# Performance work log

Measured on AMD Instinct MI355X. Metric: run time of the kernel, lower is better.

Reference implementation:

```python
import jax, jax.numpy as jnp
import numpy as np
from functools import partial

B = 524288      # batch
CH = 30         # channel_num (input dim)
FEA = 42        # feature dim consumed by all classifiers
HID = 64        # assumed hidden width of the (unshown) Feature MLP
NC = 2          # num_class -> number of conditional-domain experts
ND = 6          # num_domain
ALPHA = 1.0

# Gradient Reversal Layer: identity fwd, -alpha * grad bwd
@partial(jax.custom_vjp, nondiff_argnums=(1,))
def grl(x, alpha):
    return x

def _grl_fwd(x, alpha):
    return x, None

def _grl_bwd(alpha, res, g):
    return (-alpha * g,)

grl.defvjp(_grl_fwd, _grl_bwd)


def setup_inputs() -> dict:
    key = jax.random.key(0)
    ks = jax.random.split(key, 24)
    r = lambda k, shape, s=0.1: (jax.random.normal(k, shape, dtype=jnp.float32) * s)
    inp = {
        "x": jax.random.normal(ks[0], (B, CH), dtype=jnp.float32),
        "y": jax.random.randint(ks[1], (B,), 0, NC, dtype=jnp.int32),
        # Feature MLP (assumed: CH -> HID -> FEA with ReLU)
        "W_f1": r(ks[2], (CH, HID)), "b_f1": jnp.zeros((HID,), jnp.float32),
        "W_f2": r(ks[3], (HID, FEA)), "b_f2": jnp.zeros((FEA,), jnp.float32),
        # TaskClassifier: 42 -> 20 -> NC
        "W_t1": r(ks[4], (FEA, 20)), "b_t1": jnp.zeros((20,), jnp.float32),
        "W_t2": r(ks[5], (20, NC)), "b_t2": jnp.zeros((NC,), jnp.float32),
        # prior domain classifier: 42 -> 20 -> 20 -> ND
        "W_p1": r(ks[6], (FEA, 20)), "b_p1": jnp.zeros((20,), jnp.float32),
        "W_p2": r(ks[7], (20, 20)), "b_p2": jnp.zeros((20,), jnp.float32),
        "W_p3": r(ks[8], (20, ND)), "b_p3": jnp.zeros((ND,), jnp.float32),
        # NC conditional domain experts, stacked: [NC, ...]
        "W_c1": r(ks[9], (NC, FEA, 20)), "b_c1": jnp.zeros((NC, 20), jnp.float32),
        "W_c2": r(ks[10], (NC, 20, 20)), "b_c2": jnp.zeros((NC, 20), jnp.float32),
        "W_c3": r(ks[11], (NC, 20, ND)), "b_c3": jnp.zeros((NC, ND), jnp.float32),
    }
    return inp


def reference(x, y, W_f1, b_f1, W_f2, b_f2, W_t1, b_t1, W_t2, b_t2,
              W_p1, b_p1, W_p2, b_p2, W_p3, b_p3,
              W_c1, b_c1, W_c2, b_c2, W_c3, b_c3):
    # feature extractor
    h = jax.nn.relu(x @ W_f1 + b_f1)
    fea = jax.nn.relu(h @ W_f2 + b_f2)              # [B, 42]
    # task head
    t = jax.nn.relu(fea @ W_t1 + b_t1)
    task_predict = t @ W_t2 + b_t2                   # [B, NC]
    # gradient-reversed feature for domain heads
    fr = grl(fea, ALPHA)
    # prior domain classifier
    p = jax.nn.relu(fr @ W_p1 + b_p1)
    p = jax.nn.relu(p @ W_p2 + b_p2)
    pd_predict = p @ W_p3 + b_p3                     # [B, ND]
    # conditional experts: with NC=2 compute all experts, then route by label
    c = jax.nn.relu(jnp.einsum('bf,cfh->bch', fr, W_c1) + b_c1[None])
    c = jax.nn.relu(jnp.einsum('bch,chk->bck', c, W_c2) + b_c2[None])
    cd_all = jnp.einsum('bck,ckd->bcd', c, W_c3) + b_c3[None]   # [B, NC, ND]
    cd_predicts = jnp.take_along_axis(cd_all, y[:, None, None].astype(jnp.int32), axis=1)[:, 0, :]
    return (task_predict, pd_predict, cd_predicts)
```

## Files before the change

kernel.cpp:

```cpp
#include <hip/hip_runtime.h>
#include <hip/hip_bf16.h>

typedef __bf16 bf8 __attribute__((ext_vector_type(8)));
typedef unsigned short u16x8 __attribute__((ext_vector_type(8)));
typedef float f32x4 __attribute__((ext_vector_type(4)));
typedef float f32x2 __attribute__((ext_vector_type(2)));
typedef unsigned int u32x4 __attribute__((ext_vector_type(4)));

union FragU { u16x8 u; bf8 b; u32x4 q; };
union BiasU { f32x4 f; u32x4 q; };

struct __attribute__((packed, aligned(4))) F4u { float v[4]; };
struct __attribute__((packed, aligned(4))) F2u { float v[2]; };

static __device__ __forceinline__ f32x4 MM(const FragU& a, const FragU& b, f32x4 c) {
  return __builtin_amdgcn_mfma_f32_16x16x32_bf16(a.b, b.b, c, 0, 0, 0);
}

#define NBATCH 524288
#define NTIL (NBATCH / 128)
#define GRID 512
#define NFRAG 37

__global__ __launch_bounds__(64) void cdann_prep(
    const float* __restrict__ gWf1, const float* __restrict__ gbf1,
    const float* __restrict__ gWf2, const float* __restrict__ gbf2,
    const float* __restrict__ gWt1, const float* __restrict__ gbt1,
    const float* __restrict__ gWt2, const float* __restrict__ gbt2,
    const float* __restrict__ gWp1, const float* __restrict__ gbp1,
    const float* __restrict__ gWp2, const float* __restrict__ gbp2,
    const float* __restrict__ gWp3, const float* __restrict__ gbp3,
    const float* __restrict__ gWc1, const float* __restrict__ gbc1,
    const float* __restrict__ gWc2, const float* __restrict__ gbc2,
    const float* __restrict__ gWc3, const float* __restrict__ gbc3,
    u32x4* __restrict__ ws)
{
  const int lane = (int)threadIdx.x & 63;
  const int fid = (int)blockIdx.x;
  const int g = lane >> 4;
  const int c15 = lane & 15;

  auto colF2 = [](int nt, int m) -> int {
    if (nt < 2) return 8 * (m >> 2) + 4 * nt + (m & 3);
    const int gm = m >> 2, r = m & 3;
    if (gm == 0) return 32 + r;
    if (gm == 1) return 36 + r;
    if (gm == 2 && r < 2) return 40 + r;
    return -1;
  };

  if (fid >= 34) {
    const int nt = fid - 34;
    BiasU b;
#pragma unroll
    for (int r = 0; r < 4; ++r) {
      const int col = colF2(nt, g * 4 + r);
      b.f[r] = (col >= 0) ? gbf2[col] : 0.f;
    }
    ws[fid * 64 + lane] = b.q;
    return;
  }

  auto v_f1 = [&](int k, int m, int nt) -> float {
    const int n = 32 * (nt >> 1) + 8 * (m >> 2) + 4 * (nt & 1) + (m & 3);
    if (k < 30) return gWf1[k * 64 + n];
    if (k == 30) return gbf1[n];
    return 0.f;
  };
  auto v_f2 = [&](int k, int m, int nt) -> float {
    const int col = colF2(nt, m);
    return (col >= 0) ? gWf2[k * 42 + col] : 0.f;
  };
  auto ffea = [](int v) -> int {
    if (v < 36) return v;
    if (v == 36) return -2;
    if (v >= 40 && v <= 43) return v - 4;
    if (v == 48 || v == 49) return v - 8;
    return -1;
  };
  auto v_q = [&](int k, int m, int nt) -> float {
    const int i = ffea(k);
    if (i == -1) return 0.f;
    const int gm = m >> 2;
    const int u = 4 * nt + (m & 3);
    const int head = u / 5;
    const int f = 5 * gm + (u % 5);
    if (head == 0) return (i == -2) ? gbt1[f] : gWt1[i * 20 + f];
    if (head == 1) return (i == -2) ? gbp1[f] : gWp1[i * 20 + f];
    if (head == 2) return (i == -2) ? gbc1[f] : gWc1[i * 20 + f];
    return (i == -2) ? gbc1[20 + f] : gWc1[(42 + i) * 20 + f];
  };
  auto v_tp = [&](int k, int m, int nt) -> float {
    const int ks = k >> 5, j = k & 7, gk = (k >> 3) & 3;
    const int gm = m >> 2;
    const int u = 4 * nt + (m & 3);
    const int isP2 = (u < 5);
    const int cp = 5 * gm + u;
    const int isT2 = (!isP2 && gm == 0 && (u == 5 || u == 6));
    const int ct = u - 5;
    if (ks == 0) {
      if (j < 5) { const int i = 5 * gk + j; return isT2 ? gWt2[i * 2 + ct] : 0.f; }
      if (j == 7 && gk == 0) { if (isT2) return gbt2[ct]; if (isP2) return gbp2[cp]; }
      return 0.f;
    } else {
      if (j < 5) { const int i = 5 * gk + j; return isP2 ? gWp2[i * 20 + cp] : 0.f; }
      return 0.f;
    }
  };
  auto v_cc = [&](int k, int m, int nt) -> float {
    const int ks = k >> 5, j = k & 7, gk = (k >> 3) & 3;
    const int gm = m >> 2;
    const int u = 4 * nt + (m & 3);
    const int isE0 = (u < 5);
    const int isE1 = (u >= 5 && u < 10);
    const int c0 = 5 * gm + u;
    const int c1 = 5 * gm + (u - 5);
    if (ks == 0) {
      if (j < 5) { const int i = 5 * gk + j; return isE0 ? gWc2[i * 20 + c0] : 0.f; }
      if (j == 7 && gk == 0) { if (isE0) return gbc2[c0]; if (isE1) return gbc2[20 + c1]; }
      return 0.f;
    } else {
      if (j < 5) { const int i = 5 * gk + j; return isE1 ? gWc2[(20 + i) * 20 + c1] : 0.f; }
      return 0.f;
    }
  };
  auto v_o = [&](int k, int m, int nt) -> float {
    const int ks = k >> 5, j = k & 7, gk = (k >> 3) & 3;
    const int gm = m >> 2, r = m & 3;
    int kind = -1, c = 0;
    if (nt == 0) {
      if (gm == 0) { kind = 0; c = r; }
      else if (gm == 1) { if (r < 2) { kind = 0; c = 4 + r; } else { kind = 1; c = r - 2; } }
      else if (gm == 2) { kind = 1; c = 2 + r; }
      else { kind = 2; c = r; }
    } else {
      if (gm == 0 && r < 2) { kind = 2; c = 4 + r; }
    }
    if (kind < 0) return 0.f;
    if (ks == 0) {
      if (j < 5) { const int i = 5 * gk + j; return (kind == 0) ? gWp3[i * 6 + c] : 0.f; }
      if (j < 7) { const int i = 5 * gk + (j - 5); return (kind == 2) ? gWc3[(20 + i) * 6 + c] : 0.f; }
      if (gk == 0) {
        if (kind == 0) return gbp3[c];
        if (kind == 1) return gbc3[c];
        return gbc3[6 + c];
      }
      return 0.f;
    } else {
      if (j < 5) { const int i = 5 * gk + j; return (kind == 1) ? gWc3[i * 6 + c] : 0.f; }
      const int i = 5 * gk + 2 + (j - 5);
      return (kind == 2) ? gWc3[(20 + i) * 6 + c] : 0.f;
    }
  };

  int ks, nt, which;
  if (fid < 4)       { ks = 0;                nt = fid;            which = 0; }
  else if (fid < 10) { int t = fid - 4;  ks = t / 3; nt = t % 3;   which = 1; }
  else if (fid < 20) { int t = fid - 10; ks = t / 5; nt = t % 5;   which = 2; }
  else if (fid < 24) { int t = fid - 20; ks = t / 2; nt = t % 2;   which = 3; }
  else if (fid < 30) { int t = fid - 24; ks = t / 3; nt = t % 3;   which = 4; }
  else               { int t = fid - 30; ks = t / 2; nt = t % 2;   which = 5; }

  FragU f;
#pragma unroll
  for (int j = 0; j < 8; ++j) {
    const int k = ks * 32 + g * 8 + j;
    float v;
    switch (which) {
      case 0: v = v_f1(k, c15, nt); break;
      case 1: v = v_f2(k, c15, nt); break;
      case 2: v = v_q(k, c15, nt); break;
      case 3: v = v_tp(k, c15, nt); break;
      case 4: v = v_cc(k, c15, nt); break;
      default: v = v_o(k, c15, nt); break;
    }
    f.b[j] = (__bf16)v;
  }
  ws[fid * 64 + lane] = f.q;
}

__global__ __launch_bounds__(256, 2) void cdann_fwd(
    const float* __restrict__ gx, const int* __restrict__ gy,
    const u32x4* __restrict__ ws, float* __restrict__ gout)
{
  const int tid = (int)threadIdx.x;
  const int lane = tid & 63;
  const int w = tid >> 6;
  const int g = lane >> 4;
  const int c15 = lane & 15;

  FragU wF1[4], wF2[2][3], wQ[2][5], wTP[2][2], wCC[2][3], wO[2][2];
#pragma unroll
  for (int nt = 0; nt < 4; ++nt) wF1[nt].q = ws[nt * 64 + lane];
#pragma unroll
  for (int ks = 0; ks < 2; ++ks) {
#pragma unroll
    for (int nt = 0; nt < 3; ++nt) wF2[ks][nt].q = ws[(4 + ks * 3 + nt) * 64 + lane];
#pragma unroll
    for (int nt = 0; nt < 5; ++nt) wQ[ks][nt].q = ws[(10 + ks * 5 + nt) * 64 + lane];
#pragma unroll
    for (int nt = 0; nt < 2; ++nt) wTP[ks][nt].q = ws[(20 + ks * 2 + nt) * 64 + lane];
#pragma unroll
    for (int nt = 0; nt < 3; ++nt) wCC[ks][nt].q = ws[(24 + ks * 3 + nt) * 64 + lane];
#pragma unroll
    for (int nt = 0; nt < 2; ++nt) wO[ks][nt].q = ws[(30 + ks * 2 + nt) * 64 + lane];
  }
  f32x4 bF2[3];
#pragma unroll
  for (int nt = 0; nt < 3; ++nt) {
    BiasU b; b.q = ws[(34 + nt) * 64 + lane];
    bF2[nt] = b.f;
  }

#pragma unroll
  for (int nt = 0; nt < 4; ++nt) asm volatile("" : "+v"(wF1[nt].u));
#pragma unroll
  for (int ks = 0; ks < 2; ++ks) {
#pragma unroll
    for (int nt = 0; nt < 3; ++nt) asm volatile("" : "+v"(wF2[ks][nt].u));
#pragma unroll
    for (int nt = 0; nt < 5; ++nt) asm volatile("" : "+v"(wQ[ks][nt].u));
#pragma unroll
    for (int nt = 0; nt < 2; ++nt) asm volatile("" : "+v"(wTP[ks][nt].u));
#pragma unroll
    for (int nt = 0; nt < 3; ++nt) asm volatile("" : "+v"(wCC[ks][nt].u));
#pragma unroll
    for (int nt = 0; nt < 2; ++nt) asm volatile("" : "+v"(wO[ks][nt].u));
  }
#pragma unroll
  for (int nt = 0; nt < 3; ++nt) asm volatile("" : "+v"(bF2[nt]));

  const f32x4 zf = {0.f, 0.f, 0.f, 0.f};
  const __bf16 one = (__bf16)1.0f;
  const __bf16 zero = (__bf16)0.0f;
  float* const outT = gout;
  float* const outP = gout + (size_t)2 * NBATCH;
  float* const outC = gout + (size_t)8 * NBATCH;

  auto chain = [&](const FragU& bx, int s, int y) {
    f32x4 aH[4];
#pragma unroll
    for (int nt = 0; nt < 4; ++nt) aH[nt] = MM(wF1[nt], bx, zf);
    FragU bh0, bh1;
#pragma unroll
    for (int j = 0; j < 8; ++j) {
      bh0.b[j] = (__bf16)fmaxf(aH[j >> 2][j & 3], 0.f);
      bh1.b[j] = (__bf16)fmaxf(aH[2 + (j >> 2)][j & 3], 0.f);
    }
    f32x4 aF[3];
#pragma unroll
    for (int nt = 0; nt < 3; ++nt) aF[nt] = MM(wF2[1][nt], bh1, MM(wF2[0][nt], bh0, zf));
    FragU bf0, bf1;
#pragma unroll
    for (int j = 0; j < 8; ++j)
      bf0.b[j] = (__bf16)fmaxf(aF[j >> 2][j & 3] + bF2[j >> 2][j & 3], 0.f);
#pragma unroll
    for (int j = 0; j < 4; ++j)
      bf1.b[j] = (__bf16)fmaxf(aF[2][j] + bF2[2][j], 0.f);
    bf1.b[4] = (g == 0) ? one : zero;
    bf1.b[5] = zero; bf1.b[6] = zero; bf1.b[7] = zero;
    f32x4 aQ[5];
#pragma unroll
    for (int nt = 0; nt < 5; ++nt) aQ[nt] = MM(wQ[1][nt], bf1, MM(wQ[0][nt], bf0, zf));
    auto rq = [&](int u) { return (__bf16)fmaxf(aQ[u >> 2][u & 3], 0.f); };
    FragU tp0, tp1, cc0, cc1;
#pragma unroll
    for (int j = 0; j < 5; ++j) {
      tp0.b[j] = rq(j);
      tp1.b[j] = rq(5 + j);
      cc0.b[j] = rq(10 + j);
      cc1.b[j] = rq(15 + j);
    }
    tp0.b[5] = zero; tp0.b[6] = zero; tp0.b[7] = (g == 0) ? one : zero;
    tp1.b[5] = zero; tp1.b[6] = zero; tp1.b[7] = zero;
    cc0.b[5] = zero; cc0.b[6] = zero; cc0.b[7] = (g == 0) ? one : zero;
    cc1.b[5] = zero; cc1.b[6] = zero; cc1.b[7] = zero;
    f32x4 aT[2], aC[3];
#pragma unroll
    for (int nt = 0; nt < 2; ++nt) aT[nt] = MM(wTP[1][nt], tp1, MM(wTP[0][nt], tp0, zf));
#pragma unroll
    for (int nt = 0; nt < 3; ++nt) aC[nt] = MM(wCC[1][nt], cc1, MM(wCC[0][nt], cc0, zf));
    FragU f50, f51;
#pragma unroll
    for (int j = 0; j < 4; ++j) {
      f50.b[j] = (__bf16)fmaxf(aT[0][j], 0.f);
      f51.b[j] = (__bf16)fmaxf(aC[0][j], 0.f);
    }
    f50.b[4] = (__bf16)fmaxf(aT[1][0], 0.f);
    f50.b[5] = (__bf16)fmaxf(aC[1][1], 0.f);
    f50.b[6] = (__bf16)fmaxf(aC[1][2], 0.f);
    f50.b[7] = (g == 0) ? one : zero;
    f51.b[4] = (__bf16)fmaxf(aC[1][0], 0.f);
    f51.b[5] = (__bf16)fmaxf(aC[1][3], 0.f);
    f51.b[6] = (__bf16)fmaxf(aC[2][0], 0.f);
    f51.b[7] = (__bf16)fmaxf(aC[2][1], 0.f);
    f32x4 aO[2];
#pragma unroll
    for (int nt = 0; nt < 2; ++nt) aO[nt] = MM(wO[1][nt], f51, MM(wO[0][nt], f50, zf));
    if (g == 0) {
      f32x2 t2v = {aT[1][1], aT[1][2]};
      *(f32x2*)(outT + (size_t)s * 2) = t2v;
      f32x2 pa = {aO[0][0], aO[0][1]}, pb = {aO[0][2], aO[0][3]};
      *(f32x2*)(outP + (size_t)s * 6) = pa;
      *(f32x2*)(outP + (size_t)s * 6 + 2) = pb;
      if (y) { f32x2 cv = {aO[1][0], aO[1][1]}; *(f32x2*)(outC + (size_t)s * 6 + 4) = cv; }
    } else if (g == 1) {
      f32x2 pc = {aO[0][0], aO[0][1]};
      *(f32x2*)(outP + (size_t)s * 6 + 4) = pc;
      if (!y) { f32x2 cv = {aO[0][2], aO[0][3]}; *(f32x2*)(outC + (size_t)s * 6) = cv; }
    } else if (g == 2) {
      if (!y) {
        f32x2 ca = {aO[0][0], aO[0][1]}, cb = {aO[0][2], aO[0][3]};
        *(f32x2*)(outC + (size_t)s * 6 + 2) = ca;
        *(f32x2*)(outC + (size_t)s * 6 + 4) = cb;
      }
    } else {
      if (y) {
        f32x2 ca = {aO[0][0], aO[0][1]}, cb = {aO[0][2], aO[0][3]};
        *(f32x2*)(outC + (size_t)s * 6) = ca;
        *(f32x2*)(outC + (size_t)s * 6 + 2) = cb;
      }
    }
  };

  float xrA[8], xrB[8];
  int yA, yB;
  auto loadx = [&](int it) {
    const int sA = it * 128 + w * 16 + c15;
    const float* xpA = gx + (size_t)sA * 30 + g * 8;
    const float* xpB = xpA + (size_t)64 * 30;
    if (g < 3) {
      F4u a0 = *(const F4u*)xpA; F4u a1 = *(const F4u*)(xpA + 4);
      F4u b0 = *(const F4u*)xpB; F4u b1 = *(const F4u*)(xpB + 4);
#pragma unroll
      for (int j = 0; j < 4; ++j) {
        xrA[j] = a0.v[j]; xrA[4 + j] = a1.v[j];
        xrB[j] = b0.v[j]; xrB[4 + j] = b1.v[j];
      }
    } else {
      F4u a0 = *(const F4u*)xpA; F2u a1 = *(const F2u*)(xpA + 4);
      F4u b0 = *(const F4u*)xpB; F2u b1 = *(const F2u*)(xpB + 4);
#pragma unroll
      for (int j = 0; j < 4; ++j) { xrA[j] = a0.v[j]; xrB[j] = b0.v[j]; }
      xrA[4] = a1.v[0]; xrA[5] = a1.v[1]; xrA[6] = 1.0f; xrA[7] = 0.0f;
      xrB[4] = b1.v[0]; xrB[5] = b1.v[1]; xrB[6] = 1.0f; xrB[7] = 0.0f;
    }
    yA = gy[sA]; yB = gy[sA + 64];
  };

  int it = (int)blockIdx.x;
  loadx(it);

  while (it < NTIL) {
    const int nit = it + GRID;
    const int sgA = it * 128 + w * 16 + c15;
    const int sgB = sgA + 64;
    const int ysA = yA, ysB = yB;

    FragU bxA, bxB;
#pragma unroll
    for (int j = 0; j < 8; ++j) { bxA.b[j] = (__bf16)xrA[j]; bxB.b[j] = (__bf16)xrB[j]; }

    if (nit < NTIL) loadx(nit);

    chain(bxA, sgA, ysA);
    chain(bxB, sgB, ysB);

    it = nit;
  }
}

extern "C" void kernel_launch(void* const* d_in, const int* in_sizes, int n_in,
                              void* d_out, int out_size, void* d_ws, size_t ws_size,
                              hipStream_t stream) {
  (void)in_sizes; (void)n_in; (void)ws_size; (void)out_size;
  const float* gx  = (const float*)d_in[0];
  const int*   gy  = (const int*)d_in[1];
  const float* Wf1 = (const float*)d_in[2];  const float* bf1 = (const float*)d_in[3];
  const float* Wf2 = (const float*)d_in[4];  const float* bf2 = (const float*)d_in[5];
  const float* Wt1 = (const float*)d_in[6];  const float* bt1 = (const float*)d_in[7];
  const float* Wt2 = (const float*)d_in[8];  const float* bt2 = (const float*)d_in[9];
  const float* Wp1 = (const float*)d_in[10]; const float* bp1 = (const float*)d_in[11];
  const float* Wp2 = (const float*)d_in[12]; const float* bp2 = (const float*)d_in[13];
  const float* Wp3 = (const float*)d_in[14]; const float* bp3 = (const float*)d_in[15];
  const float* Wc1 = (const float*)d_in[16]; const float* bc1 = (const float*)d_in[17];
  const float* Wc2 = (const float*)d_in[18]; const float* bc2 = (const float*)d_in[19];
  const float* Wc3 = (const float*)d_in[20]; const float* bc3 = (const float*)d_in[21];
  float* out = (float*)d_out;
  u32x4* ws = (u32x4*)d_ws;

  cdann_prep<<<dim3(NFRAG), dim3(64), 0, stream>>>(
      Wf1, bf1, Wf2, bf2, Wt1, bt1, Wt2, bt2,
      Wp1, bp1, Wp2, bp2, Wp3, bp3, Wc1, bc1, Wc2, bc2, Wc3, bc3, ws);

  cdann_fwd<<<dim3(GRID), dim3(256), 0, stream>>>(gx, gy, ws, out);
}
```

Measured before the change: 36.29 us.

## Interleave four independent MFMA chains per stage and drop software prefetch

The main kernel now handles four 16-sample chunks per tile and runs each layer stage across all four chunks before moving to the next layer. This exposes independent MFMA chains to hide MFMA latency and dependency stalls. The cross-iteration x prefetch is replaced by loading all chunks at the top of each iteration. The grid doubles and the iteration count is fixed at compile time. Register pressure rises from keeping four chunks' fragments live, and load latency is no longer overlapped with the previous tile's compute.

```diff
diff --git a/kernel.cpp b/kernel.cpp
--- a/kernel.cpp
+++ b/kernel.cpp
@@ -18,8 +18,11 @@
 }
 
 #define NBATCH 524288
-#define NTIL (NBATCH / 128)
-#define GRID 512
+#define NCH 4
+#define SPB (NCH * 16 * 4)
+#define NTIL (NBATCH / SPB)
+#define GRID 1024
+#define ITERS (NTIL / GRID)
 #define NFRAG 37
 
 __global__ __launch_bounds__(64) void cdann_prep(
@@ -237,136 +240,137 @@
   float* const outP = gout + (size_t)2 * NBATCH;
   float* const outC = gout + (size_t)8 * NBATCH;
 
-  auto chain = [&](const FragU& bx, int s, int y) {
-    f32x4 aH[4];
-#pragma unroll
-    for (int nt = 0; nt < 4; ++nt) aH[nt] = MM(wF1[nt], bx, zf);
-    FragU bh0, bh1;
-#pragma unroll
-    for (int j = 0; j < 8; ++j) {
-      bh0.b[j] = (__bf16)fmaxf(aH[j >> 2][j & 3], 0.f);
-      bh1.b[j] = (__bf16)fmaxf(aH[2 + (j >> 2)][j & 3], 0.f);
-    }
-    f32x4 aF[3];
-#pragma unroll
-    for (int nt = 0; nt < 3; ++nt) aF[nt] = MM(wF2[1][nt], bh1, MM(wF2[0][nt], bh0, zf));
-    FragU bf0, bf1;
-#pragma unroll
-    for (int j = 0; j < 8; ++j)
-      bf0.b[j] = (__bf16)fmaxf(aF[j >> 2][j & 3] + bF2[j >> 2][j & 3], 0.f);
-#pragma unroll
-    for (int j = 0; j < 4; ++j)
-      bf1.b[j] = (__bf16)fmaxf(aF[2][j] + bF2[2][j], 0.f);
-    bf1.b[4] = (g == 0) ? one : zero;
-    bf1.b[5] = zero; bf1.b[6] = zero; bf1.b[7] = zero;
-    f32x4 aQ[5];
-#pragma unroll
-    for (int nt = 0; nt < 5; ++nt) aQ[nt] = MM(wQ[1][nt], bf1, MM(wQ[0][nt], bf0, zf));
-    auto rq = [&](int u) { return (__bf16)fmaxf(aQ[u >> 2][u & 3], 0.f); };
-    FragU tp0, tp1, cc0, cc1;
-#pragma unroll
-    for (int j = 0; j < 5; ++j) {
-      tp0.b[j] = rq(j);
-      tp1.b[j] = rq(5 + j);
-      cc0.b[j] = rq(10 + j);
-      cc1.b[j] = rq(15 + j);
-    }
-    tp0.b[5] = zero; tp0.b[6] = zero; tp0.b[7] = (g == 0) ? one : zero;
-    tp1.b[5] = zero; tp1.b[6] = zero; tp1.b[7] = zero;
-    cc0.b[5] = zero; cc0.b[6] = zero; cc0.b[7] = (g == 0) ? one : zero;
-    cc1.b[5] = zero; cc1.b[6] = zero; cc1.b[7] = zero;
-    f32x4 aT[2], aC[3];
-#pragma unroll
-    for (int nt = 0; nt < 2; ++nt) aT[nt] = MM(wTP[1][nt], tp1, MM(wTP[0][nt], tp0, zf));
-#pragma unroll
-    for (int nt = 0; nt < 3; ++nt) aC[nt] = MM(wCC[1][nt], cc1, MM(wCC[0][nt], cc0, zf));
-    FragU f50, f51;
-#pragma unroll
-    for (int j = 0; j < 4; ++j) {
-      f50.b[j] = (__bf16)fmaxf(aT[0][j], 0.f);
-      f51.b[j] = (__bf16)fmaxf(aC[0][j], 0.f);
-    }
-    f50.b[4] = (__bf16)fmaxf(aT[1][0], 0.f);
-    f50.b[5] = (__bf16)fmaxf(aC[1][1], 0.f);
-    f50.b[6] = (__bf16)fmaxf(aC[1][2], 0.f);
-    f50.b[7] = (g == 0) ? one : zero;
-    f51.b[4] = (__bf16)fmaxf(aC[1][0], 0.f);
-    f51.b[5] = (__bf16)fmaxf(aC[1][3], 0.f);
-    f51.b[6] = (__bf16)fmaxf(aC[2][0], 0.f);
-    f51.b[7] = (__bf16)fmaxf(aC[2][1], 0.f);
-    f32x4 aO[2];
-#pragma unroll
-    for (int nt = 0; nt < 2; ++nt) aO[nt] = MM(wO[1][nt], f51, MM(wO[0][nt], f50, zf));
-    if (g == 0) {
-      f32x2 t2v = {aT[1][1], aT[1][2]};
-      *(f32x2*)(outT + (size_t)s * 2) = t2v;
-      f32x2 pa = {aO[0][0], aO[0][1]}, pb = {aO[0][2], aO[0][3]};
-      *(f32x2*)(outP + (size_t)s * 6) = pa;
-      *(f32x2*)(outP + (size_t)s * 6 + 2) = pb;
-      if (y) { f32x2 cv = {aO[1][0], aO[1][1]}; *(f32x2*)(outC + (size_t)s * 6 + 4) = cv; }
-    } else if (g == 1) {
-      f32x2 pc = {aO[0][0], aO[0][1]};
-      *(f32x2*)(outP + (size_t)s * 6 + 4) = pc;
-      if (!y) { f32x2 cv = {aO[0][2], aO[0][3]}; *(f32x2*)(outC + (size_t)s * 6) = cv; }
-    } else if (g == 2) {
-      if (!y) {
-        f32x2 ca = {aO[0][0], aO[0][1]}, cb = {aO[0][2], aO[0][3]};
-        *(f32x2*)(outC + (size_t)s * 6 + 2) = ca;
-        *(f32x2*)(outC + (size_t)s * 6 + 4) = cb;
-      }
-    } else {
-      if (y) {
-        f32x2 ca = {aO[0][0], aO[0][1]}, cb = {aO[0][2], aO[0][3]};
-        *(f32x2*)(outC + (size_t)s * 6) = ca;
-        *(f32x2*)(outC + (size_t)s * 6 + 2) = cb;
-      }
-    }
-  };
-
-  float xrA[8], xrB[8];
-  int yA, yB;
-  auto loadx = [&](int it) {
-    const int sA = it * 128 + w * 16 + c15;
-    const float* xpA = gx + (size_t)sA * 30 + g * 8;
-    const float* xpB = xpA + (size_t)64 * 30;
-    if (g < 3) {
-      F4u a0 = *(const F4u*)xpA; F4u a1 = *(const F4u*)(xpA + 4);
-      F4u b0 = *(const F4u*)xpB; F4u b1 = *(const F4u*)(xpB + 4);
+  for (int ii = 0; ii < ITERS; ++ii) {
+    const int it = (int)blockIdx.x + ii * GRID;
+    const int base = it * SPB + w * (NCH * 16) + c15;
+
+    float xr[NCH][8];
+    int ys[NCH];
+#pragma unroll
+    for (int c = 0; c < NCH; ++c) {
+      const int s = base + c * 16;
+      const float* xp = gx + (size_t)s * 30 + g * 8;
+      if (g < 3) {
+        F4u a0 = *(const F4u*)xp; F4u a1 = *(const F4u*)(xp + 4);
+#pragma unroll
+        for (int j = 0; j < 4; ++j) { xr[c][j] = a0.v[j]; xr[c][4 + j] = a1.v[j]; }
+      } else {
+        F4u a0 = *(const F4u*)xp; F2u a1 = *(const F2u*)(xp + 4);
+#pragma unroll
+        for (int j = 0; j < 4; ++j) xr[c][j] = a0.v[j];
+        xr[c][4] = a1.v[0]; xr[c][5] = a1.v[1];
+        xr[c][6] = 1.0f; xr[c][7] = 0.0f;
+      }
+      ys[c] = gy[s];
+    }
+
+    FragU bh0[NCH], bh1[NCH];
+#pragma unroll
+    for (int c = 0; c < NCH; ++c) {
+      FragU bx;
+#pragma unroll
+      for (int j = 0; j < 8; ++j) bx.b[j] = (__bf16)xr[c][j];
+      f32x4 aH[4];
+#pragma unroll
+      for (int nt = 0; nt < 4; ++nt) aH[nt] = MM(wF1[nt], bx, zf);
+#pragma unroll
+      for (int j = 0; j < 8; ++j) {
+        bh0[c].b[j] = (__bf16)fmaxf(aH[j >> 2][j & 3], 0.f);
+        bh1[c].b[j] = (__bf16)fmaxf(aH[2 + (j >> 2)][j & 3], 0.f);
+      }
+    }
+
+    FragU bf0[NCH], bf1[NCH];
+#pragma unroll
+    for (int c = 0; c < NCH; ++c) {
+      f32x4 aF[3];
+#pragma unroll
+      for (int nt = 0; nt < 3; ++nt) aF[nt] = MM(wF2[1][nt], bh1[c], MM(wF2[0][nt], bh0[c], zf));
+#pragma unroll
+      for (int j = 0; j < 8; ++j)
+        bf0[c].b[j] = (__bf16)fmaxf(aF[j >> 2][j & 3] + bF2[j >> 2][j & 3], 0.f);
+#pragma unroll
+      for (int j = 0; j < 4; ++j)
+        bf1[c].b[j] = (__bf16)fmaxf(aF[2][j] + bF2[2][j], 0.f);
+      bf1[c].b[4] = (g == 0) ? one : zero;
+      bf1[c].b[5] = zero; bf1[c].b[6] = zero; bf1[c].b[7] = zero;
+    }
+
+    f32x4 aOr0[NCH], aOr1[NCH];
+    f32x2 t2v[NCH];
+#pragma unroll
+    for (int c = 0; c < NCH; ++c) {
+      f32x4 aQ[5];
+#pragma unroll
+      for (int nt = 0; nt < 5; ++nt) aQ[nt] = MM(wQ[1][nt], bf1[c], MM(wQ[0][nt], bf0[c], zf));
+      auto rq = [&](int u) { return (__bf16)fmaxf(aQ[u >> 2][u & 3], 0.f); };
+      FragU tp0, tp1, cc0, cc1;
+#pragma unroll
+      for (int j = 0; j < 5; ++j) {
+        tp0.b[j] = rq(j);
+        tp1.b[j] = rq(5 + j);
+        cc0.b[j] = rq(10 + j);
+        cc1.b[j] = rq(15 + j);
+      }
+      tp0.b[5] = zero; tp0.b[6] = zero; tp0.b[7] = (g == 0) ? one : zero;
+      tp1.b[5] = zero; tp1.b[6] = zero; tp1.b[7] = zero;
+      cc0.b[5] = zero; cc0.b[6] = zero; cc0.b[7] = (g == 0) ? one : zero;
+      cc1.b[5] = zero; cc1.b[6] = zero; cc1.b[7] = zero;
+      f32x4 aT[2], aC[3];
+#pragma unroll
+      for (int nt = 0; nt < 2; ++nt) aT[nt] = MM(wTP[1][nt], tp1, MM(wTP[0][nt], tp0, zf));
+#pragma unroll
+      for (int nt = 0; nt < 3; ++nt) aC[nt] = MM(wCC[1][nt], cc1, MM(wCC[0][nt], cc0, zf));
+      FragU f50, f51;
 #pragma unroll
       for (int j = 0; j < 4; ++j) {
-        xrA[j] = a0.v[j]; xrA[4 + j] = a1.v[j];
-        xrB[j] = b0.v[j]; xrB[4 + j] = b1.v[j];
-      }
-    } else {
-      F4u a0 = *(const F4u*)xpA; F2u a1 = *(const F2u*)(xpA + 4);
-      F4u b0 = *(const F4u*)xpB; F2u b1 = *(const F2u*)(xpB + 4);
-#pragma unroll
-      for (int j = 0; j < 4; ++j) { xrA[j] = a0.v[j]; xrB[j] = b0.v[j]; }
-      xrA[4] = a1.v[0]; xrA[5] = a1.v[1]; xrA[6] = 1.0f; xrA[7] = 0.0f;
-      xrB[4] = b1.v[0]; xrB[5] = b1.v[1]; xrB[6] = 1.0f; xrB[7] = 0.0f;
-    }
-    yA = gy[sA]; yB = gy[sA + 64];
-  };
-
-  int it = (int)blockIdx.x;
-  loadx(it);
-
-  while (it < NTIL) {
-    const int nit = it + GRID;
-    const int sgA = it * 128 + w * 16 + c15;
-    const int sgB = sgA + 64;
-    const int ysA = yA, ysB = yB;
-
-    FragU bxA, bxB;
-#pragma unroll
-    for (int j = 0; j < 8; ++j) { bxA.b[j] = (__bf16)xrA[j]; bxB.b[j] = (__bf16)xrB[j]; }
-
-    if (nit < NTIL) loadx(nit);
-
-    chain(bxA, sgA, ysA);
-    chain(bxB, sgB, ysB);
-
-    it = nit;
+        f50.b[j] = (__bf16)fmaxf(aT[0][j], 0.f);
+        f51.b[j] = (__bf16)fmaxf(aC[0][j], 0.f);
+      }
+      f50.b[4] = (__bf16)fmaxf(aT[1][0], 0.f);
+      f50.b[5] = (__bf16)fmaxf(aC[1][1], 0.f);
+      f50.b[6] = (__bf16)fmaxf(aC[1][2], 0.f);
+      f50.b[7] = (g == 0) ? one : zero;
+      f51.b[4] = (__bf16)fmaxf(aC[1][0], 0.f);
+      f51.b[5] = (__bf16)fmaxf(aC[1][3], 0.f);
+      f51.b[6] = (__bf16)fmaxf(aC[2][0], 0.f);
+      f51.b[7] = (__bf16)fmaxf(aC[2][1], 0.f);
+      aOr0[c] = MM(wO[0][0], f50, zf);
+      aOr0[c] = MM(wO[1][0], f51, aOr0[c]);
+      aOr1[c] = MM(wO[0][1], f50, zf);
+      aOr1[c] = MM(wO[1][1], f51, aOr1[c]);
+      t2v[c][0] = aT[1][1]; t2v[c][1] = aT[1][2];
+    }
+
+#pragma unroll
+    for (int c = 0; c < NCH; ++c) {
+      const int s = base + c * 16;
+      const int y = ys[c];
+      const f32x4 aO0 = aOr0[c], aO1 = aOr1[c];
+      if (g == 0) {
+        *(f32x2*)(outT + (size_t)s * 2) = t2v[c];
+        f32x2 pa = {aO0[0], aO0[1]}, pb = {aO0[2], aO0[3]};
+        *(f32x2*)(outP + (size_t)s * 6) = pa;
+        *(f32x2*)(outP + (size_t)s * 6 + 2) = pb;
+        if (y) { f32x2 cv = {aO1[0], aO1[1]}; *(f32x2*)(outC + (size_t)s * 6 + 4) = cv; }
+      } else if (g == 1) {
+        f32x2 pc = {aO0[0], aO0[1]};
+        *(f32x2*)(outP + (size_t)s * 6 + 4) = pc;
+        if (!y) { f32x2 cv = {aO0[2], aO0[3]}; *(f32x2*)(outC + (size_t)s * 6) = cv; }
+      } else if (g == 2) {
+        if (!y) {
+          f32x2 ca = {aO0[0], aO0[1]}, cb = {aO0[2], aO0[3]};
+          *(f32x2*)(outC + (size_t)s * 6 + 2) = ca;
+          *(f32x2*)(outC + (size_t)s * 6 + 4) = cb;
+        }
+      } else {
+        if (y) {
+          f32x2 ca = {aO0[0], aO0[1]}, cb = {aO0[2], aO0[3]};
+          *(f32x2*)(outC + (size_t)s * 6) = ca;
+          *(f32x2*)(outC + (size_t)s * 6 + 2) = cb;
+        }
+      }
+    }
   }
 }
 
```

Measured after the change: 41.38 us. 1.14x slower.
